# Performance work log

Measured on AMD Instinct MI355X. Metric: run time of the kernel, lower is better.

The kernel has to match this reference:

```python
import jax, jax.numpy as jnp
import numpy as np

D_MODEL = 1024
N_HEADS = 16
D_K = D_MODEL // N_HEADS
THETA = 10000.0
B, S = 2, 2048


def setup_inputs() -> dict:
    key = jax.random.key(0)
    ks = jax.random.split(key, 5)
    sigma = 2.0 / (D_MODEL + D_MODEL) ** 0.5
    x = jax.random.normal(ks[0], (B, S, D_MODEL), dtype=jnp.float32)
    Wq = jax.random.normal(ks[1], (D_MODEL, D_MODEL), dtype=jnp.float32) * sigma
    Wk = jax.random.normal(ks[2], (D_MODEL, D_MODEL), dtype=jnp.float32) * sigma
    Wv = jax.random.normal(ks[3], (D_MODEL, D_MODEL), dtype=jnp.float32) * sigma
    Wo = jax.random.normal(ks[4], (D_MODEL, D_MODEL), dtype=jnp.float32) * sigma
    token_positions = jnp.arange(S, dtype=jnp.int64 if jax.config.read('jax_enable_x64') else jnp.int32)
    return {"x": x, "Wq": Wq, "Wk": Wk, "Wv": Wv, "Wo": Wo, "token_positions": token_positions}


def _apply_rope(t, token_positions):
    # t: (H, B, S, D_K); token_positions: (S,) broadcasts over leading dims
    half = D_K // 2
    inv_freq = 1.0 / (THETA ** (jnp.arange(0, D_K, 2, dtype=jnp.float32) / D_K))  # (half,)
    ang = token_positions.astype(jnp.float32)[..., None] * inv_freq              # (S, half)
    cos, sin = jnp.cos(ang), jnp.sin(ang)
    t2 = t.reshape(*t.shape[:-1], half, 2)  # interleaved pairs
    o0 = t2[..., 0] * cos - t2[..., 1] * sin
    o1 = t2[..., 0] * sin + t2[..., 1] * cos
    return jnp.stack((o0, o1), axis=-1).reshape(t.shape)


def _split_heads(t):
    # (B, S, D_MODEL) -> (H, B, S, D_K)
    Bb, Ss, _ = t.shape
    return jnp.moveaxis(t.reshape(Bb, Ss, N_HEADS, D_K), 2, 0)


def reference(x, Wq, Wk, Wv, Wo, token_positions):
    Q = _split_heads(jnp.einsum('oi,bsi->bso', Wq, x))
    K = _split_heads(jnp.einsum('oi,bsi->bso', Wk, x))
    V = _split_heads(jnp.einsum('oi,bsi->bso', Wv, x))
    Q = _apply_rope(Q, token_positions)
    K = _apply_rope(K, token_positions)
    scores = jnp.einsum('hbqd,hbkd->hbqk', Q, K) * (D_K ** -0.5)  # (H,B,S,S)
    causal = jnp.tril(jnp.ones((S, S), dtype=bool))
    scores = jnp.where(causal, scores, -jnp.inf)
    attn = jax.nn.softmax(scores, axis=-1)
    out = jnp.einsum('hbqk,hbkd->hbqd', attn, V)  # (H,B,S,D_K)
    out = jnp.moveaxis(out, 0, 2).reshape(x.shape[0], x.shape[1], D_MODEL)
    return jnp.einsum('oi,bsi->bso', Wo, out)
```

## Files before the change

### kernel.cpp

```cpp
#include <hip/hip_runtime.h>

#define DM 1024
#define NH 16
#define DK 64
#define BB 2
#define SS 2048

typedef unsigned short u16;
typedef unsigned int   u32;
typedef __bf16 bf16x8 __attribute__((ext_vector_type(8)));
typedef float  f32x4  __attribute__((ext_vector_type(4)));

__device__ __forceinline__ u16 f2bf(float f){
  u32 u = __float_as_uint(f);
  u32 r = (u + 0x7FFFu + ((u >> 16) & 1u)) >> 16;
  return (u16)r;
}
__device__ __forceinline__ float bf2f(u16 v){ return __uint_as_float(((u32)v) << 16); }

__device__ __forceinline__ u32 cvtpk(float lo, float hi){
  u32 r;
  asm volatile("v_cvt_pk_bf16_f32 %0, %1, %2" : "=v"(r) : "v"(lo), "v"(hi));
  return r;
}

__device__ __forceinline__ void gl16(const void* g, void* l){
  __builtin_amdgcn_global_load_lds((const __attribute__((address_space(1))) u32*)g,
                                   (__attribute__((address_space(3))) u32*)l, 16, 0, 0);
}
__device__ __forceinline__ f32x4 mfma16(bf16x8 a, bf16x8 b, f32x4 c){
  return __builtin_amdgcn_mfma_f32_16x16x32_bf16(a, b, c, 0, 0, 0);
}

__global__ void k_cast(const float* __restrict__ x,  const float* __restrict__ wq,
                       const float* __restrict__ wk, const float* __restrict__ wv,
                       const float* __restrict__ wo, u16* __restrict__ xb,
                       u16* __restrict__ wb, float* __restrict__ tab){
  if (blockIdx.x >= 8192){
    int e = (blockIdx.x - 8192)*256 + threadIdx.x;
    int p = e >> 5, j = e & 31;
    float s, c;
    sincosf((float)p * exp2f(-0.4152410118609203f * (float)j), &s, &c);
    float2 v; v.x = c; v.y = s;
    *(float2*)(tab + e*2) = v;
    return;
  }
  int e = blockIdx.x*1024 + threadIdx.x*4;
  int r = e >> 20;
  const float* s; u16* d; int local;
  if (r < 4){ s = x; d = xb; local = e; }
  else {
    const float* ws[4] = {wq, wk, wv, wo};
    int w = r - 4;
    local = e & 0xFFFFF;
    s = ws[w]; d = wb + ((size_t)w << 20);
  }
  float4 v = *(const float4*)(s + local);
  uint2 t; t.x = cvtpk(v.x, v.y); t.y = cvtpk(v.z, v.w);
  *(uint2*)(d + local) = t;
}

__device__ __forceinline__ int xcd_swz(int lin, int nwg){
  return (lin & 7) * (nwg >> 3) + (lin >> 3);
}

template<bool SWAP>
__device__ __forceinline__ void gemm_core(const u16* __restrict__ A, const u16* __restrict__ Bw,
                                          u16* S, f32x4 (&acc)[4][4], int m0, int n0){
  const int tid = threadIdx.x, lane = tid & 63, wid = tid >> 6;
  const int wm = (wid >> 1) * 64, wn = (wid & 1) * 64;
  const int ql = lane & 15, lg = lane >> 4;

  #define STAGE_G(buf, k0)                                                       \
    _Pragma("unroll")                                                            \
    for (int i = 0; i < 4; i++){                                                 \
      int L = i*4096 + tid*16;                                                   \
      int r_ = L >> 7;                                                           \
      int orig = ((L >> 4) & 7) ^ (r_ & 7);                                      \
      const u16* src = (orig < 4)                                                \
          ? (A  + (size_t)(m0 + r_)*DM + (k0) + orig*8)                          \
          : (Bw + (size_t)(n0 + r_)*DM + (k0) + (orig - 4)*8);                   \
      gl16(src, (char*)(buf) + L);                                               \
    }

  #define COMPUTE_T(buf)                                                         \
    {                                                                            \
      bf16x8 af[4], bfr[4];                                                      \
      _Pragma("unroll")                                                          \
      for (int mi = 0; mi < 4; mi++){                                            \
        int r = wm + mi*16 + ql;                                                 \
        af[mi] = *(const bf16x8*)((char*)(buf) + r*128 + ((lg*16) ^ ((r & 7) << 4))); \
      }                                                                          \
      _Pragma("unroll")                                                          \
      for (int ni = 0; ni < 4; ni++){                                            \
        int r = wn + ni*16 + ql;                                                 \
        bfr[ni] = *(const bf16x8*)((char*)(buf) + r*128 + ((64 + lg*16) ^ ((r & 7) << 4))); \
      }                                                                          \
      __builtin_amdgcn_s_setprio(1);                                             \
      _Pragma("unroll")                                                          \
      for (int mi = 0; mi < 4; mi++)                                             \
        _Pragma("unroll")                                                        \
        for (int ni = 0; ni < 4; ni++)                                           \
          acc[mi][ni] = SWAP ? mfma16(bfr[ni], af[mi], acc[mi][ni])              \
                             : mfma16(af[mi], bfr[ni], acc[mi][ni]);             \
      __builtin_amdgcn_s_setprio(0);                                             \
    }

  char* b0 = (char*)S;
  char* b1 = (char*)S + 16384;
  char* b2 = (char*)S + 32768;

  STAGE_G(b0, 0);
  STAGE_G(b1, 32);

  #pragma unroll 3
  for (int t = 0; t < 30; t++){
    asm volatile("s_waitcnt vmcnt(4)" ::: "memory");
    __builtin_amdgcn_s_barrier();
    STAGE_G(b2, (t+2)*32);
    COMPUTE_T(b0);
    char* tmp = b0; b0 = b1; b1 = b2; b2 = tmp;
  }
  asm volatile("s_waitcnt vmcnt(4)" ::: "memory");
  __builtin_amdgcn_s_barrier();
  COMPUTE_T(b0);
  { char* tmp = b0; b0 = b1; b1 = b2; b2 = tmp; }
  asm volatile("s_waitcnt vmcnt(0)" ::: "memory");
  __builtin_amdgcn_s_barrier();
  COMPUTE_T(b0);

  #undef STAGE_G
  #undef COMPUTE_T
}

__global__ __launch_bounds__(256) void k_gemm_qkv(const u16* __restrict__ xb, const u16* __restrict__ Wb,
                                                  u16* __restrict__ Qb, u16* __restrict__ Kb,
                                                  u16* __restrict__ Vt_g, const int* __restrict__ pos,
                                                  const float* __restrict__ tab){
  __shared__ __align__(16) u16 S[3*8192];
  int lin = (int)blockIdx.x + 8*((int)blockIdx.y + 32*(int)blockIdx.z);
  lin = xcd_swz(lin, 768);
  const int bx = lin & 7, by = (lin >> 3) & 31, z = lin >> 8;
  const int m0 = by * 128, n0 = bx * 128;

  const u16* Bw = Wb + ((size_t)z << 20);
  f32x4 acc[4][4] = {};
  gemm_core<true>(xb, Bw, S, acc, m0, n0);
  const int lane = threadIdx.x & 63, wid = threadIdx.x >> 6;
  const int wm0 = m0 + (wid >> 1)*64, wn0 = n0 + (wid & 1)*64;
  const int ql = lane & 15, lg = lane >> 4;

  if (z == 2){
    #pragma unroll
    for (int mi = 0; mi < 4; mi++){
      const int mrow = wm0 + mi*16 + ql;
      const int bq = mrow >> 11, sq = mrow & (SS-1);
      u16* vt = Vt_g + ((size_t)bq*NH*DK)*SS + sq;
      #pragma unroll
      for (int ni = 0; ni < 4; ni++){
        const int nb = wn0 + ni*16 + lg*4;
        #pragma unroll
        for (int r = 0; r < 4; r++)
          vt[(size_t)(nb + r)*SS] = f2bf(acc[mi][ni][r]);
      }
    }
    return;
  }

  u16* C = (z == 0) ? Qb : Kb;
  const float4* tab4 = (const float4*)tab;
  #pragma unroll
  for (int mi = 0; mi < 4; mi++){
    const int mrow = wm0 + mi*16 + ql;
    const int p = pos[mrow & (SS-1)];
    #pragma unroll
    for (int ni = 0; ni < 4; ni++){
      const int nb = wn0 + ni*16 + lg*4;
      float o0 = acc[mi][ni][0], o1 = acc[mi][ni][1];
      float o2 = acc[mi][ni][2], o3 = acc[mi][ni][3];
      int j0 = (nb >> 1) & 31;
      float4 cs = tab4[p*16 + (j0 >> 1)];
      float t0 = o0*cs.x - o1*cs.y, t1 = o0*cs.y + o1*cs.x;
      o0 = t0; o1 = t1;
      t0 = o2*cs.z - o3*cs.w; t1 = o2*cs.w + o3*cs.z;
      o2 = t0; o3 = t1;
      uint2 w; w.x = cvtpk(o0, o1); w.y = cvtpk(o2, o3);
      *(uint2*)(C + (size_t)mrow*DM + nb) = w;
    }
  }
}

__global__ __launch_bounds__(256) void k_gemm_out(const u16* __restrict__ AO, const u16* __restrict__ Wo,
                                                  float* __restrict__ Co){
  __shared__ __align__(16) u16 S[3*8192];
  int lin = (int)blockIdx.x + 8*(int)blockIdx.y;
  lin = xcd_swz(lin, 256);
  const int bx = lin & 7, by = lin >> 3;
  const int m0 = by * 128, n0 = bx * 128;

  f32x4 acc[4][4] = {};
  gemm_core<false>(AO, Wo, S, acc, m0, n0);
  const int lane = threadIdx.x & 63, wid = threadIdx.x >> 6;
  const int wm0 = m0 + (wid >> 1)*64, wn0 = n0 + (wid & 1)*64;
  #pragma unroll
  for (int mi = 0; mi < 4; mi++)
    #pragma unroll
    for (int ni = 0; ni < 4; ni++)
      #pragma unroll
      for (int r = 0; r < 4; r++){
        int m = wm0 + mi*16 + (lane >> 4)*4 + r;
        int n = wn0 + ni*16 + (lane & 15);
        Co[(size_t)m*DM + n] = acc[mi][ni][r];
      }
}

__global__ __launch_bounds__(512) void k_attn(const u16* __restrict__ Q, const u16* __restrict__ K,
                                              const u16* __restrict__ Vt_g, u16* __restrict__ AO){
  __shared__ __align__(16) u16 Ks[3][64*64];
  __shared__ __align__(16) u16 Vt[3][64*64];
  __shared__ __align__(16) u16 Ps[8][16*64];
  const int tid = threadIdx.x, lane = tid & 63, wid = tid >> 6;
  const int b = blockIdx.z, h = blockIdx.y;
  const int qb = b ? (15 - (int)blockIdx.x) : (int)blockIdx.x;
  const int qw = qb*128 + wid*16;
  const size_t base = ((size_t)b*SS)*DM + (size_t)h*DK;
  const size_t vtb  = ((size_t)b*NH + h)*DK*SS;
  const int ql = lane & 15, lg = lane >> 4;
  const int NT = 2*qb + 2;

  const u16* qptr = Q + base + (size_t)(qw + ql)*DM + lg*8;
  bf16x8 qf0 = *(const bf16x8*)(qptr);
  bf16x8 qf1 = *(const bf16x8*)(qptr + 32);

  f32x4 oacc[4] = {};
  float m = -3e38f, lsum = 0.f;
  const float SC = 0.18033688011112042f;
  const float THR = 8.0f / SC;

  const int srow = tid >> 3;
  const int sin = ((tid & 7) * 16) ^ ((srow & 7) << 4);

  #define STAGE_A(bi, t)                                                          \
    {                                                                             \
      const int kn0_ = (t)*64;                                                    \
      gl16(K    + base + (size_t)(kn0_ + srow)*DM + (sin >> 1), (char*)Ks[bi] + tid*16); \
      gl16(Vt_g + vtb  + (size_t)srow*SS + kn0_ + (sin >> 1), (char*)Vt[bi] + tid*16);   \
    }

  STAGE_A(0, 0);
  STAGE_A(1, 1);
  asm volatile("s_waitcnt vmcnt(2)" ::: "memory");
  __builtin_amdgcn_s_barrier();

  int c0 = 0, c1 = 1, c2 = 2;
  for (int kt = 0; kt < NT; kt++){
    const int kv0 = kt*64;
    const bool have2 = (kt + 2 < NT);
    if (have2) STAGE_A(c2, kt + 2);

    const bool active = (kv0 <= qw + 15);
    if (active){
      f32x4 sf[4] = {};
      __builtin_amdgcn_s_setprio(1);
      #pragma unroll
      for (int kk = 0; kk < 2; kk++){
        const int co = kk*64 + lg*16;
        #pragma unroll
        for (int f = 0; f < 4; f++){
          int kvr = f*16 + ql;
          bf16x8 kf = *(const bf16x8*)((const char*)Ks[c0] + ((kvr*128 + co) ^ ((kvr & 7) << 4)));
          sf[f] = mfma16(kf, kk ? qf1 : qf0, sf[f]);
        }
      }
      __builtin_amdgcn_s_setprio(0);

      if (kv0 + 63 > qw){
        const int qa = qw + ql;
        #pragma unroll
        for (int f = 0; f < 4; f++)
          #pragma unroll
          for (int r = 0; r < 4; r++){
            int kva = kv0 + f*16 + lg*4 + r;
            sf[f][r] = (kva <= qa) ? sf[f][r] : -3e38f;
          }
      }

      float mx01 = fmaxf(fmaxf(sf[0][0], sf[0][1]), fmaxf(sf[0][2], sf[0][3]));
      float mx23 = fmaxf(fmaxf(sf[1][0], sf[1][1]), fmaxf(sf[1][2], sf[1][3]));
      float mx45 = fmaxf(fmaxf(sf[2][0], sf[2][1]), fmaxf(sf[2][2], sf[2][3]));
      float mx67 = fmaxf(fmaxf(sf[3][0], sf[3][1]), fmaxf(sf[3][2], sf[3][3]));
      float mx = fmaxf(fmaxf(mx01, mx23), fmaxf(mx45, mx67));

      if (!__all(mx <= m + THR)){
        mx = fmaxf(mx, __shfl_xor(mx, 16));
        mx = fmaxf(mx, __shfl_xor(mx, 32));
        const float mn = fmaxf(m, mx);
        const float alpha = exp2f((m - mn)*SC);
        #pragma unroll
        for (int ni = 0; ni < 4; ni++) oacc[ni] *= alpha;
        lsum *= alpha;
        m = mn;
      }

      const float nms = -m*SC;
      float p[4][4];
      float psum = 0.f;
      #pragma unroll
      for (int f = 0; f < 4; f++)
        #pragma unroll
        for (int r = 0; r < 4; r++){
          p[f][r] = exp2f(fmaf(sf[f][r], SC, nms));
          psum += p[f][r];
        }
      lsum += psum;

      #pragma unroll
      for (int f = 0; f < 4; f++)
        #pragma unroll
        for (int r = 0; r < 4; r += 2){
          int kv = f*16 + lg*4 + r;
          int byteoff = (ql*128 + kv*2) ^ ((ql & 7) << 4);
          *(u32*)((char*)Ps[wid] + byteoff) = cvtpk(p[f][r], p[f][r+1]);
        }

      __builtin_amdgcn_s_setprio(1);
      #pragma unroll
      for (int kk = 0; kk < 2; kk++){
        bf16x8 pf = *(const bf16x8*)((const char*)Ps[wid] +
                      ((ql*128 + kk*64 + lg*16) ^ ((ql & 7) << 4)));
        #pragma unroll
        for (int ni = 0; ni < 4; ni++){
          int d = ni*16 + ql;
          bf16x8 vf = *(const bf16x8*)((const char*)Vt[c0] +
                        ((d*128 + kk*64 + lg*16) ^ ((d & 7) << 4)));
          oacc[ni] = mfma16(vf, pf, oacc[ni]);
        }
      }
      __builtin_amdgcn_s_setprio(0);
    }

    if (kt + 1 < NT){
      if (have2) asm volatile("s_waitcnt vmcnt(2)" ::: "memory");
      else       asm volatile("s_waitcnt vmcnt(0)" ::: "memory");
      __builtin_amdgcn_s_barrier();
    }
    int tmp = c0; c0 = c1; c1 = c2; c2 = tmp;
  }
  #undef STAGE_A

  lsum += __shfl_xor(lsum, 16);
  lsum += __shfl_xor(lsum, 32);
  const float rl = 1.0f / lsum;
  #pragma unroll
  for (int ni = 0; ni < 4; ni++)
    #pragma unroll
    for (int r = 0; r < 4; r += 2){
      int d = ni*16 + lg*4 + r;
      int byteoff = (ql*128 + d*2) ^ ((ql & 7) << 4);
      *(u32*)((char*)Ps[wid] + byteoff) = cvtpk(oacc[ni][r]*rl, oacc[ni][r+1]*rl);
    }
  #pragma unroll
  for (int pass = 0; pass < 2; pass++){
    int qr = pass*8 + (lane >> 3);
    int d0 = (lane & 7)*8;
    bf16x8 row = *(const bf16x8*)((const char*)Ps[wid] + ((qr*128 + d0*2) ^ ((qr & 7) << 4)));
    *(bf16x8*)(AO + base + (size_t)(qw + qr)*DM + d0) = row;
  }
}

extern "C" void kernel_launch(void* const* d_in, const int* in_sizes, int n_in,
                              void* d_out, int out_size, void* d_ws, size_t ws_size,
                              hipStream_t stream){
  const float* x   = (const float*)d_in[0];
  const float* Wq  = (const float*)d_in[1];
  const float* Wk  = (const float*)d_in[2];
  const float* Wv  = (const float*)d_in[3];
  const float* Wo  = (const float*)d_in[4];
  const int*   pos = (const int*)d_in[5];
  float* out = (float*)d_out;

  const size_t NEED = ((size_t)41 << 20);
  if (ws_size < NEED){
    hipMemsetAsync(d_out, 0x7f, (size_t)out_size * sizeof(float), stream);
    return;
  }

  char* ws = (char*)d_ws;
  u16* xb   = (u16*)(ws);
  u16* Wb   = (u16*)(ws + ((size_t)8  << 20));
  u16* Qb   = (u16*)(ws + ((size_t)16 << 20));
  u16* Kb   = (u16*)(ws + ((size_t)24 << 20));
  u16* Vt   = (u16*)(ws + ((size_t)32 << 20));
  float* tab = (float*)(ws + ((size_t)40 << 20));
  u16* AO = xb;

  k_cast<<<8448, 256, 0, stream>>>(x, Wq, Wk, Wv, Wo, xb, Wb, tab);
  k_gemm_qkv<<<dim3(8, 32, 3), 256, 0, stream>>>(xb, Wb, Qb, Kb, Vt, pos, tab);
  k_attn<<<dim3(16, 16, 2), 512, 0, stream>>>(Qb, Kb, Vt, AO);
  k_gemm_out<<<dim3(8, 32), 256, 0, stream>>>(AO, Wb + ((size_t)3 << 20), out);
}
```

Measured before the change: 118.2 us.

## Double attention KV tile to 128 keys per pipeline stage

The causal flash-attention kernel now processes 128 keys per iteration instead of 64. This halves the loop trip count, barriers and online-softmax rescale checks, and it issues two global-to-LDS loads per thread per stage. The per-warp activity check is dropped because every tile now overlaps the query block. The P tile, the Vt tile and the output staging switch to 256-byte swizzled rows with wider packed stores. The shared-memory footprint roughly doubles to about 128 KB, which likely limits the kernel to one block per CU and reduces latency hiding.

```diff
diff --git a/kernel.cpp b/kernel.cpp
--- a/kernel.cpp
+++ b/kernel.cpp
@@ -216,9 +216,9 @@
 
 __global__ __launch_bounds__(512) void k_attn(const u16* __restrict__ Q, const u16* __restrict__ K,
                                               const u16* __restrict__ Vt_g, u16* __restrict__ AO){
-  __shared__ __align__(16) u16 Ks[3][64*64];
-  __shared__ __align__(16) u16 Vt[3][64*64];
-  __shared__ __align__(16) u16 Ps[8][16*64];
+  __shared__ __align__(16) u16 Ks[3][128*64];
+  __shared__ __align__(16) u16 Vt[3][64*128];
+  __shared__ __align__(16) u16 Ps[8][16*128];
   const int tid = threadIdx.x, lane = tid & 63, wid = tid >> 6;
   const int b = blockIdx.z, h = blockIdx.y;
   const int qb = b ? (15 - (int)blockIdx.x) : (int)blockIdx.x;
@@ -226,7 +226,7 @@
   const size_t base = ((size_t)b*SS)*DM + (size_t)h*DK;
   const size_t vtb  = ((size_t)b*NH + h)*DK*SS;
   const int ql = lane & 15, lg = lane >> 4;
-  const int NT = 2*qb + 2;
+  const int NT = qb + 1;
 
   const u16* qptr = Q + base + (size_t)(qw + ql)*DM + lg*8;
   bf16x8 qf0 = *(const bf16x8*)(qptr);
@@ -236,111 +236,112 @@
   float m = -3e38f, lsum = 0.f;
   const float SC = 0.18033688011112042f;
   const float THR = 8.0f / SC;
-
-  const int srow = tid >> 3;
-  const int sin = ((tid & 7) * 16) ^ ((srow & 7) << 4);
+  const int qswz = (ql & 7) << 4;
 
   #define STAGE_A(bi, t)                                                          \
     {                                                                             \
-      const int kn0_ = (t)*64;                                                    \
-      gl16(K    + base + (size_t)(kn0_ + srow)*DM + (sin >> 1), (char*)Ks[bi] + tid*16); \
-      gl16(Vt_g + vtb  + (size_t)srow*SS + kn0_ + (sin >> 1), (char*)Vt[bi] + tid*16);   \
+      const int kn0_ = (t)*128;                                                   \
+      _Pragma("unroll")                                                           \
+      for (int i_ = 0; i_ < 2; i_++){                                             \
+        int L = i_*8192 + tid*16;                                                 \
+        int rK = L >> 7;                                                          \
+        int iK = (L & 127) ^ ((rK & 7) << 4);                                     \
+        gl16(K + base + (size_t)(kn0_ + rK)*DM + (iK >> 1), (char*)Ks[bi] + L);   \
+        int rV = L >> 8;                                                          \
+        int iV = (L & 255) ^ ((rV & 7) << 4);                                     \
+        gl16(Vt_g + vtb + (size_t)rV*SS + kn0_ + (iV >> 1), (char*)Vt[bi] + L);   \
+      }                                                                           \
     }
 
   STAGE_A(0, 0);
-  STAGE_A(1, 1);
-  asm volatile("s_waitcnt vmcnt(2)" ::: "memory");
+  STAGE_A(1, (NT > 1) ? 1 : 0);
+  asm volatile("s_waitcnt vmcnt(4)" ::: "memory");
   __builtin_amdgcn_s_barrier();
 
   int c0 = 0, c1 = 1, c2 = 2;
   for (int kt = 0; kt < NT; kt++){
-    const int kv0 = kt*64;
+    const int kv0 = kt*128;
     const bool have2 = (kt + 2 < NT);
     if (have2) STAGE_A(c2, kt + 2);
 
-    const bool active = (kv0 <= qw + 15);
-    if (active){
-      f32x4 sf[4] = {};
-      __builtin_amdgcn_s_setprio(1);
-      #pragma unroll
-      for (int kk = 0; kk < 2; kk++){
-        const int co = kk*64 + lg*16;
-        #pragma unroll
-        for (int f = 0; f < 4; f++){
-          int kvr = f*16 + ql;
-          bf16x8 kf = *(const bf16x8*)((const char*)Ks[c0] + ((kvr*128 + co) ^ ((kvr & 7) << 4)));
-          sf[f] = mfma16(kf, kk ? qf1 : qf0, sf[f]);
-        }
+    f32x4 sf[8] = {};
+    __builtin_amdgcn_s_setprio(1);
+    #pragma unroll
+    for (int kk = 0; kk < 2; kk++){
+      const int co = kk*64 + lg*16;
+      #pragma unroll
+      for (int f = 0; f < 8; f++){
+        int kvr = f*16 + ql;
+        bf16x8 kf = *(const bf16x8*)((const char*)Ks[c0] + ((kvr*128 + co) ^ ((kvr & 7) << 4)));
+        sf[f] = mfma16(kf, kk ? qf1 : qf0, sf[f]);
       }
-      __builtin_amdgcn_s_setprio(0);
-
-      if (kv0 + 63 > qw){
-        const int qa = qw + ql;
-        #pragma unroll
-        for (int f = 0; f < 4; f++)
-          #pragma unroll
-          for (int r = 0; r < 4; r++){
-            int kva = kv0 + f*16 + lg*4 + r;
-            sf[f][r] = (kva <= qa) ? sf[f][r] : -3e38f;
-          }
-      }
-
-      float mx01 = fmaxf(fmaxf(sf[0][0], sf[0][1]), fmaxf(sf[0][2], sf[0][3]));
-      float mx23 = fmaxf(fmaxf(sf[1][0], sf[1][1]), fmaxf(sf[1][2], sf[1][3]));
-      float mx45 = fmaxf(fmaxf(sf[2][0], sf[2][1]), fmaxf(sf[2][2], sf[2][3]));
-      float mx67 = fmaxf(fmaxf(sf[3][0], sf[3][1]), fmaxf(sf[3][2], sf[3][3]));
-      float mx = fmaxf(fmaxf(mx01, mx23), fmaxf(mx45, mx67));
-
-      if (!__all(mx <= m + THR)){
-        mx = fmaxf(mx, __shfl_xor(mx, 16));
-        mx = fmaxf(mx, __shfl_xor(mx, 32));
-        const float mn = fmaxf(m, mx);
-        const float alpha = exp2f((m - mn)*SC);
-        #pragma unroll
-        for (int ni = 0; ni < 4; ni++) oacc[ni] *= alpha;
-        lsum *= alpha;
-        m = mn;
-      }
-
-      const float nms = -m*SC;
-      float p[4][4];
-      float psum = 0.f;
-      #pragma unroll
-      for (int f = 0; f < 4; f++)
+    }
+    __builtin_amdgcn_s_setprio(0);
+
+    if (kv0 + 127 > qw){
+      const int qa = qw + ql;
+      #pragma unroll
+      for (int f = 0; f < 8; f++)
         #pragma unroll
         for (int r = 0; r < 4; r++){
-          p[f][r] = exp2f(fmaf(sf[f][r], SC, nms));
-          psum += p[f][r];
+          int kva = kv0 + f*16 + lg*4 + r;
+          sf[f][r] = (kva <= qa) ? sf[f][r] : -3e38f;
         }
-      lsum += psum;
-
-      #pragma unroll
-      for (int f = 0; f < 4; f++)
-        #pragma unroll
-        for (int r = 0; r < 4; r += 2){
-          int kv = f*16 + lg*4 + r;
-          int byteoff = (ql*128 + kv*2) ^ ((ql & 7) << 4);
-          *(u32*)((char*)Ps[wid] + byteoff) = cvtpk(p[f][r], p[f][r+1]);
-        }
-
-      __builtin_amdgcn_s_setprio(1);
-      #pragma unroll
-      for (int kk = 0; kk < 2; kk++){
-        bf16x8 pf = *(const bf16x8*)((const char*)Ps[wid] +
-                      ((ql*128 + kk*64 + lg*16) ^ ((ql & 7) << 4)));
-        #pragma unroll
-        for (int ni = 0; ni < 4; ni++){
-          int d = ni*16 + ql;
-          bf16x8 vf = *(const bf16x8*)((const char*)Vt[c0] +
-                        ((d*128 + kk*64 + lg*16) ^ ((d & 7) << 4)));
-          oacc[ni] = mfma16(vf, pf, oacc[ni]);
-        }
+    }
+
+    float mxf[8];
+    #pragma unroll
+    for (int f = 0; f < 8; f++)
+      mxf[f] = fmaxf(fmaxf(sf[f][0], sf[f][1]), fmaxf(sf[f][2], sf[f][3]));
+    float mx = fmaxf(fmaxf(fmaxf(mxf[0], mxf[1]), fmaxf(mxf[2], mxf[3])),
+                     fmaxf(fmaxf(mxf[4], mxf[5]), fmaxf(mxf[6], mxf[7])));
+
+    if (!__all(mx <= m + THR)){
+      mx = fmaxf(mx, __shfl_xor(mx, 16));
+      mx = fmaxf(mx, __shfl_xor(mx, 32));
+      const float mn = fmaxf(m, mx);
+      const float alpha = exp2f((m - mn)*SC);
+      #pragma unroll
+      for (int ni = 0; ni < 4; ni++) oacc[ni] *= alpha;
+      lsum *= alpha;
+      m = mn;
+    }
+
+    const float nms = -m*SC;
+    float p[8][4];
+    float psum = 0.f;
+    #pragma unroll
+    for (int f = 0; f < 8; f++)
+      #pragma unroll
+      for (int r = 0; r < 4; r++){
+        p[f][r] = exp2f(fmaf(sf[f][r], SC, nms));
+        psum += p[f][r];
       }
-      __builtin_amdgcn_s_setprio(0);
-    }
+    lsum += psum;
+
+    #pragma unroll
+    for (int f = 0; f < 8; f++){
+      int byteoff = (ql*256 + f*32 + lg*8) ^ qswz;
+      uint2 w; w.x = cvtpk(p[f][0], p[f][1]); w.y = cvtpk(p[f][2], p[f][3]);
+      *(uint2*)((char*)Ps[wid] + byteoff) = w;
+    }
+
+    __builtin_amdgcn_s_setprio(1);
+    #pragma unroll
+    for (int kc = 0; kc < 4; kc++){
+      const int co = kc*64 + lg*16;
+      bf16x8 pf = *(const bf16x8*)((const char*)Ps[wid] + ((ql*256 + co) ^ qswz));
+      #pragma unroll
+      for (int ni = 0; ni < 4; ni++){
+        int d = ni*16 + ql;
+        bf16x8 vf = *(const bf16x8*)((const char*)Vt[c0] + ((d*256 + co) ^ ((d & 7) << 4)));
+        oacc[ni] = mfma16(vf, pf, oacc[ni]);
+      }
+    }
+    __builtin_amdgcn_s_setprio(0);
 
     if (kt + 1 < NT){
-      if (have2) asm volatile("s_waitcnt vmcnt(2)" ::: "memory");
+      if (have2) asm volatile("s_waitcnt vmcnt(4)" ::: "memory");
       else       asm volatile("s_waitcnt vmcnt(0)" ::: "memory");
       __builtin_amdgcn_s_barrier();
     }
@@ -352,18 +353,18 @@
   lsum += __shfl_xor(lsum, 32);
   const float rl = 1.0f / lsum;
   #pragma unroll
-  for (int ni = 0; ni < 4; ni++)
-    #pragma unroll
-    for (int r = 0; r < 4; r += 2){
-      int d = ni*16 + lg*4 + r;
-      int byteoff = (ql*128 + d*2) ^ ((ql & 7) << 4);
-      *(u32*)((char*)Ps[wid] + byteoff) = cvtpk(oacc[ni][r]*rl, oacc[ni][r+1]*rl);
-    }
+  for (int ni = 0; ni < 4; ni++){
+    int byteoff = (ql*256 + (ni*16 + lg*4)*2) ^ qswz;
+    uint2 w;
+    w.x = cvtpk(oacc[ni][0]*rl, oacc[ni][1]*rl);
+    w.y = cvtpk(oacc[ni][2]*rl, oacc[ni][3]*rl);
+    *(uint2*)((char*)Ps[wid] + byteoff) = w;
+  }
   #pragma unroll
   for (int pass = 0; pass < 2; pass++){
     int qr = pass*8 + (lane >> 3);
     int d0 = (lane & 7)*8;
-    bf16x8 row = *(const bf16x8*)((const char*)Ps[wid] + ((qr*128 + d0*2) ^ ((qr & 7) << 4)));
+    bf16x8 row = *(const bf16x8*)((const char*)Ps[wid] + ((qr*256 + d0*2) ^ ((qr & 7) << 4)));
     *(bf16x8*)(AO + base + (size_t)(qw + qr)*DM + d0) = row;
   }
 }
```

Result: slower. 133.7 us (+13.1%).
